# Optimization experiments

Hardware: AMD Instinct MI355X
Metric: run time of the kernel (lower is better)

## Reference

```python
import jax, jax.numpy as jnp
import numpy as np
from jax import lax

B, S, D, H, W = 4, 4096, 512, 8, 32
LL, LG = 4, 3
HD = D // H
SF = 4   # sparsity_factor
K = 7    # depthwise conv kernel


def _ln(x, g, b):
    mu = x.mean(-1, keepdims=True)
    v = ((x - mu) ** 2).mean(-1, keepdims=True)
    return (x - mu) * lax.rsqrt(v + 1e-5) * g + b


def _mha(x, wqkv, bqkv, wp, bp, bias=None):
    Bx, Sx, Dx = x.shape
    qkv = (x @ wqkv + bqkv).reshape(Bx, Sx, 3, H, HD)
    q, k, v = jnp.moveaxis(qkv, 2, 0)          # each [B,S,H,hd]
    att = jnp.einsum('bqhd,bkhd->bhqk', q, k) * (HD ** -0.5)
    if bias is not None:
        att = att + bias                        # relative position bias [1,H,W,W]
    a = jax.nn.softmax(att, axis=-1)
    o = jnp.einsum('bhqk,bkhd->bqhd', a, v).reshape(Bx, Sx, Dx)
    return o @ wp + bp


def _ffn(x, w1, b1, w2, b2):
    return jax.nn.gelu(x @ w1 + b1) @ w2 + b2


def _dwconv(x, w, b):
    # x [B,S,D], w [D,K] depthwise, 'same' padding
    y = lax.conv_general_dilated(
        x.transpose(0, 2, 1), w[:, None, :], (1,), [((K - 1) // 2, (K - 1) // 2)],
        feature_group_count=D, dimension_numbers=('NCH', 'OIH', 'NCH'))
    return (y + b[:, None]).transpose(0, 2, 1)


def _lin_interp(x, L_out):
    # torch F.interpolate(mode='linear', align_corners=False); x [B,Lin,D]
    Lin = x.shape[1]
    pos = jnp.clip((jnp.arange(L_out, dtype=jnp.float32) + 0.5) * (Lin / L_out) - 0.5,
                   0.0, Lin - 1)
    i0 = jnp.floor(pos).astype(jnp.int32)
    i1 = jnp.minimum(i0 + 1, Lin - 1)
    w = (pos - i0)[None, :, None]
    return x[:, i0] * (1.0 - w) + x[:, i1] * w


_rel_idx = np.arange(W)[:, None] - np.arange(W)[None, :] + W - 1   # [W,W]


def _local_attn(x, wqkv, bqkv, wp, bp, rel):
    # Swin-style non-overlapping window attention with relative position bias
    NW = S // W
    bias = rel[_rel_idx].transpose(2, 0, 1)[None]   # [1,H,W,W]
    xw = x.reshape(B * NW, W, D)
    return _mha(xw, wqkv, bqkv, wp, bp, bias).reshape(B, S, D)


def _global_attn(x, wqkv, bqkv, wp, bp):
    # strided sparse global attention + linear interpolation back to S
    if S > SF * 32:
        stride = max(1, S // (SF * 32))
        xs = x[:, ::stride]                         # [B, 128, D]
        return _lin_interp(_mha(xs, wqkv, bqkv, wp, bp), S)
    return _mha(x, wqkv, bqkv, wp, bp)


def _forward(x, p):
    (lqkv_w, lqkv_b, lproj_w, lproj_b, lrel, lconv_w, lconv_b,
     ln1_g, ln1_b, lffn_w1, lffn_b1, lffn_w2, lffn_b2, ln2_g, ln2_b,
     gqkv_w, gqkv_b, gproj_w, gproj_b, gn1_g, gn1_b,
     gffn_w1, gffn_b1, gffn_w2, gffn_b2, gn2_g, gn2_b,
     fw_local, fw_global, fn_g, fn_b) = p
    # local branch: window attention + depthwise conv + FFN, pre-sum/post-norm
    xl = x
    for i in range(LL):
        a = _local_attn(xl, lqkv_w[i], lqkv_b[i], lproj_w[i], lproj_b[i], lrel[i])
        xl = _ln(xl + a, ln1_g[i], ln1_b[i])
        xl = xl + _dwconv(xl, lconv_w[i], lconv_b[i])
        f = _ffn(xl, lffn_w1[i], lffn_b1[i], lffn_w2[i], lffn_b2[i])
        xl = _ln(xl + f, ln2_g[i], ln2_b[i])
    # global branch: sparse strided attention + FFN
    xg = x
    for i in range(LG):
        a = _global_attn(xg, gqkv_w[i], gqkv_b[i], gproj_w[i], gproj_b[i])
        xg = _ln(xg + a, gn1_g[i], gn1_b[i])
        f = _ffn(xg, gffn_w1[i], gffn_b1[i], gffn_w2[i], gffn_b2[i])
        xg = _ln(xg + f, gn2_g[i], gn2_b[i])
    # weighted_sum branch fusion + LayerNorm
    w = jax.nn.softmax(jnp.stack([fw_local, fw_global]))
    return _ln(w[0] * xl + w[1] * xg, fn_g, fn_b)


def setup_inputs() -> dict:
    ks = iter(jax.random.split(jax.random.key(0), 48))
    def r(shape, s=0.02):
        return jax.random.normal(next(ks), shape, dtype=jnp.float32) * s
    return {
        'x': jax.random.normal(next(ks), (B, S, D), dtype=jnp.float32),
        'lqkv_w': r((LL, D, 3 * D)), 'lqkv_b': jnp.zeros((LL, 3 * D)),
        'lproj_w': r((LL, D, D)), 'lproj_b': jnp.zeros((LL, D)),
        'lrel': r((LL, 2 * W - 1, H)),
        'lconv_w': r((LL, D, K)), 'lconv_b': jnp.zeros((LL, D)),
        'ln1_g': jnp.ones((LL, D)), 'ln1_b': jnp.zeros((LL, D)),
        'lffn_w1': r((LL, D, 4 * D)), 'lffn_b1': jnp.zeros((LL, 4 * D)),
        'lffn_w2': r((LL, 4 * D, D)), 'lffn_b2': jnp.zeros((LL, D)),
        'ln2_g': jnp.ones((LL, D)), 'ln2_b': jnp.zeros((LL, D)),
        'gqkv_w': r((LG, D, 3 * D)), 'gqkv_b': jnp.zeros((LG, 3 * D)),
        'gproj_w': r((LG, D, D)), 'gproj_b': jnp.zeros((LG, D)),
        'gn1_g': jnp.ones((LG, D)), 'gn1_b': jnp.zeros((LG, D)),
        'gffn_w1': r((LG, D, 4 * D)), 'gffn_b1': jnp.zeros((LG, 4 * D)),
        'gffn_w2': r((LG, 4 * D, D)), 'gffn_b2': jnp.zeros((LG, D)),
        'gn2_g': jnp.ones((LG, D)), 'gn2_b': jnp.zeros((LG, D)),
        'fw_local': jnp.float32(0.5), 'fw_global': jnp.float32(0.5),
        'fn_g': jnp.ones((D,)), 'fn_b': jnp.zeros((D,)),
    }


def reference(x, lqkv_w, lqkv_b, lproj_w, lproj_b, lrel, lconv_w, lconv_b,
              ln1_g, ln1_b, lffn_w1, lffn_b1, lffn_w2, lffn_b2, ln2_g, ln2_b,
              gqkv_w, gqkv_b, gproj_w, gproj_b, gn1_g, gn1_b,
              gffn_w1, gffn_b1, gffn_w2, gffn_b2, gn2_g, gn2_b,
              fw_local, fw_global, fn_g, fn_b):
    return _forward(x, (lqkv_w, lqkv_b, lproj_w, lproj_b, lrel, lconv_w, lconv_b,
                        ln1_g, ln1_b, lffn_w1, lffn_b1, lffn_w2, lffn_b2, ln2_g, ln2_b,
                        gqkv_w, gqkv_b, gproj_w, gproj_b, gn1_g, gn1_b,
                        gffn_w1, gffn_b1, gffn_w2, gffn_b2, gn2_g, gn2_b,
                        fw_local, fw_global, fn_g, fn_b))
```

## Files before the change

kernel.cpp:

```cpp
#include <hip/hip_runtime.h>
#include <hip/hip_bf16.h>
#include <math.h>

typedef __attribute__((ext_vector_type(8))) short short8;
typedef __attribute__((ext_vector_type(4))) float float4_t;
typedef __attribute__((ext_vector_type(4))) unsigned int uint4_t;
typedef __attribute__((ext_vector_type(2))) unsigned int uint2_t;

#define DEV static __device__ __forceinline__

DEV unsigned short f2b(float f) {
    union { float f; unsigned int u; } x; x.f = f;
    unsigned int r = x.u + 0x7fffu + ((x.u >> 16) & 1u);
    return (unsigned short)(r >> 16);
}
DEV float b2f(unsigned short u) {
    union { unsigned int u; float f; } x; x.u = ((unsigned int)u) << 16;
    return x.f;
}
DEV unsigned int f2b2(float lo, float hi) {
    union { __hip_bfloat162 h; unsigned int u; } c;
    c.h = __float22bfloat162_rn(make_float2(lo, hi));
    return c.u;
}
DEV float gelu_f(float x) {
    const float a = -2.3022082f, b = -0.10294372f;
    float x2 = x * x;
    float p = __builtin_fmaf(x2, b, a);
    float e = __builtin_amdgcn_exp2f(p * x);
    return x * __builtin_amdgcn_rcpf(1.0f + e);
}

DEV void gld16(unsigned short* lds, const unsigned short* g) {
    __builtin_amdgcn_global_load_lds(
        (const __attribute__((address_space(1))) unsigned int*)g,
        (__attribute__((address_space(3))) unsigned int*)lds,
        16, 0, 0);
}

__global__ __launch_bounds__(256) void transpose_cast_batch_kernel(
    const float* __restrict__ srcL, const float* __restrict__ srcG, int nl,
    unsigned short* __restrict__ dst0, size_t perL, int Kd, int Nd)
{
    const int z = blockIdx.z;
    const float* W = (z < nl) ? srcL + (size_t)z * Kd * Nd
                              : srcG + (size_t)(z - nl) * Kd * Nd;
    unsigned short* WT = dst0 + (size_t)z * perL;
    __shared__ float tile[32][33];
    int n0 = blockIdx.x * 32, k0 = blockIdx.y * 32;
    int tx = threadIdx.x & 31, ty = threadIdx.x >> 5;
    #pragma unroll
    for (int r = ty; r < 32; r += 8)
        tile[r][tx] = W[(size_t)(k0 + r) * Nd + n0 + tx];
    __syncthreads();
    #pragma unroll
    for (int r = ty; r < 32; r += 8)
        WT[(size_t)(n0 + r) * Kd + k0 + tx] = f2b(tile[tx][r]);
}

__global__ __launch_bounds__(256) void copy_cast_kernel(
    const float* __restrict__ x, float* __restrict__ xl, float* __restrict__ xg,
    unsigned short* __restrict__ xb, int n4)
{
    int i = blockIdx.x * 256 + threadIdx.x;
    if (i < n4) {
        float4_t v = ((const float4_t*)x)[i];
        ((float4_t*)xl)[i] = v;
        ((float4_t*)xg)[i] = v;
        uint2_t p = { f2b2(v[0], v[1]), f2b2(v[2], v[3]) };
        ((uint2_t*)xb)[i] = p;
    }
}

template<int BN>
__global__ __launch_bounds__(256, 4) void gemm_db_kernel(
    const unsigned short* __restrict__ A,
    const unsigned short* __restrict__ BT,
    const float* __restrict__ bias,
    const float* __restrict__ residual,
    float* __restrict__ Cf,
    unsigned short* __restrict__ Cb,
    int M, int N, int K, int act)
{
    constexpr int NI = (BN == 128) ? 4 : 2;
    __shared__ __align__(16) unsigned short As[2][128 * 32];
    __shared__ __align__(16) unsigned short Bs[2][BN * 32];
    const int tid = threadIdx.x;
    const int wave = tid >> 6, lane = tid & 63;
    const int quad = lane >> 4, l16 = lane & 15;
    const int m0 = blockIdx.x * 128, n0 = blockIdx.y * BN;
    const int wm = (BN == 128) ? (wave >> 1) * 64 : wave * 32;
    const int wn = (BN == 128) ? (wave & 1) * 64 : 0;

    float4_t acc[NI][4] = {};

    const int lrow = lane >> 2;
    const int lcol = (lane & 3) * 8;
    const int r0 = wave * 16 + lrow;
    const unsigned short* Ag0 = A  + (size_t)(m0 + r0) * K + lcol;
    const unsigned short* Ag1 = A  + (size_t)(m0 + 64 + r0) * K + lcol;
    const unsigned short* Bg0 = BT + (size_t)(n0 + r0) * K + lcol;
    const unsigned short* Bg1 = (BN == 128) ? BT + (size_t)(n0 + 64 + r0) * K + lcol : nullptr;
    const int soff = (wave * 16) * 32 + lane * 8;

    const int iters = K >> 5;
    gld16(&As[0][soff], Ag0);
    gld16(&As[0][soff + 64 * 32], Ag1);
    gld16(&Bs[0][soff], Bg0);
    if (BN == 128) gld16(&Bs[0][soff + 64 * 32], Bg1);
    __syncthreads();

    for (int k = 0; k < iters; k++) {
        const int cur = k & 1;
        if (k + 1 < iters) {
            const int koff = (k + 1) << 5;
            const int nxt = cur ^ 1;
            gld16(&As[nxt][soff], Ag0 + koff);
            gld16(&As[nxt][soff + 64 * 32], Ag1 + koff);
            gld16(&Bs[nxt][soff], Bg0 + koff);
            if (BN == 128) gld16(&Bs[nxt][soff + 64 * 32], Bg1 + koff);
        }
        short8 a[NI], b[4];
        #pragma unroll
        for (int i = 0; i < NI; i++)
            a[i] = *(const short8*)(&As[cur][(wm + i * 16 + l16) * 32 + quad * 8]);
        #pragma unroll
        for (int j = 0; j < 4; j++)
            b[j] = *(const short8*)(&Bs[cur][(wn + j * 16 + l16) * 32 + quad * 8]);
        #pragma unroll
        for (int i = 0; i < NI; i++)
            #pragma unroll
            for (int j = 0; j < 4; j++)
                acc[i][j] = __builtin_amdgcn_mfma_f32_16x16x32_bf16(b[j], a[i], acc[i][j], 0, 0, 0);
        __syncthreads();
    }

    #pragma unroll
    for (int i = 0; i < NI; i++) {
        const int row = m0 + wm + i * 16 + l16;
        #pragma unroll
        for (int j = 0; j < 4; j++) {
            const int col = n0 + wn + j * 16 + quad * 4;
            const size_t idx = (size_t)row * N + col;
            float4_t v = acc[i][j] + *(const float4_t*)(bias + col);
            if (act == 1) {
                #pragma unroll
                for (int r = 0; r < 4; r++) v[r] = gelu_f(v[r]);
            }
            if (residual) v += *(const float4_t*)(residual + idx);
            if (Cf) *(float4_t*)(Cf + idx) = v;
            if (Cb) {
                uint2_t o = { f2b2(v[0], v[1]), f2b2(v[2], v[3]) };
                *(uint2_t*)(Cb + idx) = o;
            }
        }
    }
}

__global__ __launch_bounds__(256) void ln_kernel(
    const float* __restrict__ X, const float* __restrict__ g, const float* __restrict__ b,
    float* __restrict__ Yf, unsigned short* __restrict__ Yb)
{
    const int row = blockIdx.x * 4 + (threadIdx.x >> 6);
    const int lane = threadIdx.x & 63;
    const float* xr = X + (size_t)row * 512 + lane * 8;
    float4_t v0 = *(const float4_t*)(xr);
    float4_t v1 = *(const float4_t*)(xr + 4);
    float s = v0[0] + v0[1] + v0[2] + v0[3] + v1[0] + v1[1] + v1[2] + v1[3];
    #pragma unroll
    for (int m = 32; m > 0; m >>= 1) s += __shfl_xor(s, m);
    float mu = s * (1.0f / 512.0f);
    float4_t d0 = v0 - mu, d1 = v1 - mu;
    float s2 = d0[0]*d0[0] + d0[1]*d0[1] + d0[2]*d0[2] + d0[3]*d0[3]
             + d1[0]*d1[0] + d1[1]*d1[1] + d1[2]*d1[2] + d1[3]*d1[3];
    #pragma unroll
    for (int m = 32; m > 0; m >>= 1) s2 += __shfl_xor(s2, m);
    float rs = rsqrtf(s2 * (1.0f / 512.0f) + 1e-5f);
    float4_t g0 = *(const float4_t*)(g + lane * 8);
    float4_t g1 = *(const float4_t*)(g + lane * 8 + 4);
    float4_t b0 = *(const float4_t*)(b + lane * 8);
    float4_t b1 = *(const float4_t*)(b + lane * 8 + 4);
    float4_t y0 = d0 * rs * g0 + b0;
    float4_t y1 = d1 * rs * g1 + b1;
    if (Yf) {
        float* yr = Yf + (size_t)row * 512 + lane * 8;
        *(float4_t*)(yr) = y0;
        *(float4_t*)(yr + 4) = y1;
    }
    if (Yb) {
        uint4_t pk = { f2b2(y0[0], y0[1]), f2b2(y0[2], y0[3]),
                       f2b2(y1[0], y1[1]), f2b2(y1[2], y1[3]) };
        *(uint4_t*)(Yb + (size_t)row * 512 + lane * 8) = pk;
    }
}

__global__ __launch_bounds__(256) void interp_ln_kernel(
    const float* __restrict__ GA, float* __restrict__ XG,
    const float* __restrict__ g, const float* __restrict__ b,
    unsigned short* __restrict__ Yb)
{
    const int row = blockIdx.x * 4 + (threadIdx.x >> 6);
    const int lane = threadIdx.x & 63;
    const int bb = row >> 12, sfull = row & 4095;
    float pos = (sfull + 0.5f) * (128.0f / 4096.0f) - 0.5f;
    pos = fminf(fmaxf(pos, 0.0f), 127.0f);
    int i0 = (int)floorf(pos);
    int i1 = min(i0 + 1, 127);
    float w = pos - (float)i0;
    const float* ga0 = GA + ((size_t)bb * 128 + i0) * 512 + lane * 8;
    const float* ga1 = GA + ((size_t)bb * 128 + i1) * 512 + lane * 8;
    float* xr = XG + (size_t)row * 512 + lane * 8;
    float4_t v0 = *(const float4_t*)(xr)     + *(const float4_t*)(ga0)     * (1.0f - w) + *(const float4_t*)(ga1)     * w;
    float4_t v1 = *(const float4_t*)(xr + 4) + *(const float4_t*)(ga0 + 4) * (1.0f - w) + *(const float4_t*)(ga1 + 4) * w;
    float s = v0[0] + v0[1] + v0[2] + v0[3] + v1[0] + v1[1] + v1[2] + v1[3];
    #pragma unroll
    for (int m = 32; m > 0; m >>= 1) s += __shfl_xor(s, m);
    float mu = s * (1.0f / 512.0f);
    float4_t d0 = v0 - mu, d1 = v1 - mu;
    float s2 = d0[0]*d0[0] + d0[1]*d0[1] + d0[2]*d0[2] + d0[3]*d0[3]
             + d1[0]*d1[0] + d1[1]*d1[1] + d1[2]*d1[2] + d1[3]*d1[3];
    #pragma unroll
    for (int m = 32; m > 0; m >>= 1) s2 += __shfl_xor(s2, m);
    float rs = rsqrtf(s2 * (1.0f / 512.0f) + 1e-5f);
    float4_t g0 = *(const float4_t*)(g + lane * 8);
    float4_t g1 = *(const float4_t*)(g + lane * 8 + 4);
    float4_t b0 = *(const float4_t*)(b + lane * 8);
    float4_t b1 = *(const float4_t*)(b + lane * 8 + 4);
    float4_t y0 = d0 * rs * g0 + b0;
    float4_t y1 = d1 * rs * g1 + b1;
    *(float4_t*)(xr) = y0;
    *(float4_t*)(xr + 4) = y1;
    uint4_t pk = { f2b2(y0[0], y0[1]), f2b2(y0[2], y0[3]),
                   f2b2(y1[0], y1[1]), f2b2(y1[2], y1[3]) };
    *(uint4_t*)(Yb + (size_t)row * 512 + lane * 8) = pk;
}

__global__ __launch_bounds__(256) void local_attn_kernel(
    const unsigned short* __restrict__ QKV, const float* __restrict__ rel,
    unsigned short* __restrict__ OUT)
{
    const int blk = blockIdx.x;
    const int h = blk & 7;
    const int win = (blk >> 3) & 127;
    const int b = blk >> 10;
    const int rowbase = b * 4096 + win * 32;
    __shared__ float q[32][64], k[32][65], v[32][64];
    __shared__ float sc[32][33];
    const int tid = threadIdx.x;
    const int i = tid >> 3, c = tid & 7;
    {
        const unsigned short* base = QKV + (size_t)(rowbase + i) * 1536 + h * 64 + c * 8;
        short8 qv = *(const short8*)(base);
        short8 kv = *(const short8*)(base + 512);
        short8 vv = *(const short8*)(base + 1024);
        #pragma unroll
        for (int r = 0; r < 8; r++) {
            q[i][c * 8 + r] = b2f((unsigned short)qv[r]);
            k[i][c * 8 + r] = b2f((unsigned short)kv[r]);
            v[i][c * 8 + r] = b2f((unsigned short)vv[r]);
        }
    }
    __syncthreads();
    #pragma unroll
    for (int p = 0; p < 4; p++) {
        int idx = tid + p * 256;
        int si = idx >> 5, sj = idx & 31;
        float s = 0.f;
        #pragma unroll
        for (int d = 0; d < 64; d++) s += q[si][d] * k[sj][d];
        sc[si][sj] = s * 0.125f + rel[(si - sj + 31) * 8 + h];
    }
    __syncthreads();
    {
        const int j0 = c * 4;
        float a0 = sc[i][j0], a1 = sc[i][j0 + 1], a2 = sc[i][j0 + 2], a3 = sc[i][j0 + 3];
        float mx = fmaxf(fmaxf(a0, a1), fmaxf(a2, a3));
        #pragma unroll
        for (int m = 1; m < 8; m <<= 1) mx = fmaxf(mx, __shfl_xor(mx, m));
        float e0 = __expf(a0 - mx), e1 = __expf(a1 - mx), e2 = __expf(a2 - mx), e3 = __expf(a3 - mx);
        float sum = e0 + e1 + e2 + e3;
        #pragma unroll
        for (int m = 1; m < 8; m <<= 1) sum += __shfl_xor(sum, m);
        float inv = 1.0f / sum;
        sc[i][j0] = e0 * inv; sc[i][j0 + 1] = e1 * inv; sc[i][j0 + 2] = e2 * inv; sc[i][j0 + 3] = e3 * inv;
    }
    __syncthreads();
    float o[8] = {};
    #pragma unroll
    for (int j = 0; j < 32; j++) {
        float a = sc[i][j];
        #pragma unroll
        for (int r = 0; r < 8; r++) o[r] += a * v[j][c * 8 + r];
    }
    uint4_t pk = { f2b2(o[0], o[1]), f2b2(o[2], o[3]), f2b2(o[4], o[5]), f2b2(o[6], o[7]) };
    *(uint4_t*)(OUT + (size_t)(rowbase + i) * 512 + h * 64 + c * 8) = pk;
}

__global__ __launch_bounds__(256) void gather_xs_kernel(
    const float* __restrict__ XG, unsigned short* __restrict__ XSB)
{
    int i = blockIdx.x * 256 + threadIdx.x;
    if (i < 65536) {
        int dv = (i & 127) * 4, t = (i >> 7) & 127, b = i >> 14;
        float4_t v = *(const float4_t*)(XG + ((size_t)b * 4096 + t * 32) * 512 + dv);
        uint2_t p = { f2b2(v[0], v[1]), f2b2(v[2], v[3]) };
        *(uint2_t*)(XSB + (size_t)i * 4) = p;
    }
}

__global__ __launch_bounds__(256) void global_attn_kernel(
    const unsigned short* __restrict__ GQKV, unsigned short* __restrict__ GOUT)
{
    const int blk = blockIdx.x;
    const int qt = blk & 3, h = (blk >> 2) & 7, b = blk >> 5;
    __shared__ unsigned short ks[128 * 64], vs[128 * 64];
    __shared__ float qs[32 * 64];
    __shared__ float sc[32 * 128];
    const int tid = threadIdx.x;
    for (int idx = tid; idx < 128 * 64; idx += 256) {
        int j = idx >> 6, d = idx & 63;
        const unsigned short* rowp = GQKV + (size_t)(b * 128 + j) * 1536 + h * 64 + d;
        ks[idx] = rowp[512];
        vs[idx] = rowp[1024];
    }
    for (int idx = tid; idx < 32 * 64; idx += 256) {
        int i = idx >> 6, d = idx & 63;
        qs[idx] = b2f(GQKV[(size_t)(b * 128 + qt * 32 + i) * 1536 + h * 64 + d]);
    }
    __syncthreads();
    for (int idx = tid; idx < 32 * 128; idx += 256) {
        int i = idx >> 7, j = idx & 127;
        float s = 0.f;
        #pragma unroll
        for (int d = 0; d < 64; d++) s += qs[i * 64 + d] * b2f(ks[j * 64 + d]);
        sc[idx] = s * 0.125f;
    }
    __syncthreads();
    if (tid < 32) {
        float mx = -1e30f;
        for (int j = 0; j < 128; j++) mx = fmaxf(mx, sc[tid * 128 + j]);
        float sum = 0.f;
        for (int j = 0; j < 128; j++) { float e = __expf(sc[tid * 128 + j] - mx); sc[tid * 128 + j] = e; sum += e; }
        float inv = 1.0f / sum;
        for (int j = 0; j < 128; j++) sc[tid * 128 + j] *= inv;
    }
    __syncthreads();
    for (int idx = tid; idx < 32 * 64; idx += 256) {
        int i = idx >> 6, d = idx & 63;
        float o = 0.f;
        for (int j = 0; j < 128; j++) o += sc[i * 128 + j] * b2f(vs[j * 64 + d]);
        GOUT[(size_t)(b * 128 + qt * 32 + i) * 512 + h * 64 + d] = f2b(o);
    }
}

__global__ __launch_bounds__(256) void dwconv_add_kernel(
    const float* __restrict__ X, const float* __restrict__ wconv, const float* __restrict__ bconv,
    float* __restrict__ Yf, unsigned short* __restrict__ Yb)
{
    __shared__ float wT[7][512];
    const int tid = threadIdx.x;
    for (int idx = tid; idx < 3584; idx += 256) {
        int d = idx / 7, t = idx - d * 7;
        wT[t][d] = wconv[idx];
    }
    __syncthreads();
    const int b = blockIdx.y;
    const int s0 = blockIdx.x * 16 + (tid >> 7) * 8;
    const int dv = (tid & 127) * 4;
    const float* Xb = X + ((size_t)b * 4096) * 512 + dv;

    float4_t win[14];
    #pragma unroll
    for (int j = 0; j < 14; j++) {
        int ss = s0 - 3 + j;
        win[j] = (ss >= 0 && ss < 4096) ? *(const float4_t*)(Xb + (size_t)ss * 512)
                                        : (float4_t){0.f, 0.f, 0.f, 0.f};
    }
    float4_t bias = *(const float4_t*)(bconv + dv);
    float4_t w[7];
    #pragma unroll
    for (int t = 0; t < 7; t++) w[t] = *(const float4_t*)(&wT[t][dv]);

    #pragma unroll
    for (int j = 0; j < 8; j++) {
        float4_t acc = bias;
        #pragma unroll
        for (int t = 0; t < 7; t++) acc += win[j + t] * w[t];
        float4_t v = win[j + 3] + acc;
        size_t e = ((size_t)b * 4096 + s0 + j) * 512 + dv;
        *(float4_t*)(Yf + e) = v;
        uint2_t o = { f2b2(v[0], v[1]), f2b2(v[2], v[3]) };
        *(uint2_t*)(Yb + e) = o;
    }
}

__global__ __launch_bounds__(256) void final_kernel(
    const float* __restrict__ XL, const float* __restrict__ XG,
    const float* __restrict__ fwl, const float* __restrict__ fwg,
    const float* __restrict__ g, const float* __restrict__ bb, float* __restrict__ out)
{
    const int row = blockIdx.x * 4 + (threadIdx.x >> 6);
    const int lane = threadIdx.x & 63;
    float a = fwl[0], cc = fwg[0];
    float m = fmaxf(a, cc);
    float ea = __expf(a - m), ec = __expf(cc - m);
    float w0 = ea / (ea + ec), w1 = ec / (ea + ec);
    const float* xlr = XL + (size_t)row * 512 + lane * 8;
    const float* xgr = XG + (size_t)row * 512 + lane * 8;
    float4_t v0 = *(const float4_t*)(xlr)     * w0 + *(const float4_t*)(xgr)     * w1;
    float4_t v1 = *(const float4_t*)(xlr + 4) * w0 + *(const float4_t*)(xgr + 4) * w1;
    float s = v0[0] + v0[1] + v0[2] + v0[3] + v1[0] + v1[1] + v1[2] + v1[3];
    #pragma unroll
    for (int mm = 32; mm > 0; mm >>= 1) s += __shfl_xor(s, mm);
    float mu = s * (1.0f / 512.0f);
    float4_t d0 = v0 - mu, d1 = v1 - mu;
    float s2 = d0[0]*d0[0] + d0[1]*d0[1] + d0[2]*d0[2] + d0[3]*d0[3]
             + d1[0]*d1[0] + d1[1]*d1[1] + d1[2]*d1[2] + d1[3]*d1[3];
    #pragma unroll
    for (int mm = 32; mm > 0; mm >>= 1) s2 += __shfl_xor(s2, mm);
    float rs = rsqrtf(s2 * (1.0f / 512.0f) + 1e-5f);
    float4_t g0 = *(const float4_t*)(g + lane * 8);
    float4_t g1 = *(const float4_t*)(g + lane * 8 + 4);
    float4_t b0 = *(const float4_t*)(bb + lane * 8);
    float4_t b1 = *(const float4_t*)(bb + lane * 8 + 4);
    float* orow = out + (size_t)row * 512 + lane * 8;
    *(float4_t*)(orow)     = d0 * rs * g0 + b0;
    *(float4_t*)(orow + 4) = d1 * rs * g1 + b1;
}

extern "C" void kernel_launch(void* const* d_in, const int* in_sizes, int n_in,
                              void* d_out, int out_size, void* d_ws, size_t ws_size,
                              hipStream_t stream)
{
    (void)in_sizes; (void)n_in; (void)out_size; (void)ws_size;
    const float* x       = (const float*)d_in[0];
    const float* lqkv_w  = (const float*)d_in[1];
    const float* lqkv_b  = (const float*)d_in[2];
    const float* lproj_w = (const float*)d_in[3];
    const float* lproj_b = (const float*)d_in[4];
    const float* lrel    = (const float*)d_in[5];
    const float* lconv_w = (const float*)d_in[6];
    const float* lconv_b = (const float*)d_in[7];
    const float* ln1_g   = (const float*)d_in[8];
    const float* ln1_b   = (const float*)d_in[9];
    const float* lffn_w1 = (const float*)d_in[10];
    const float* lffn_b1 = (const float*)d_in[11];
    const float* lffn_w2 = (const float*)d_in[12];
    const float* lffn_b2 = (const float*)d_in[13];
    const float* ln2_g   = (const float*)d_in[14];
    const float* ln2_b   = (const float*)d_in[15];
    const float* gqkv_w  = (const float*)d_in[16];
    const float* gqkv_b  = (const float*)d_in[17];
    const float* gproj_w = (const float*)d_in[18];
    const float* gproj_b = (const float*)d_in[19];
    const float* gn1_g   = (const float*)d_in[20];
    const float* gn1_b   = (const float*)d_in[21];
    const float* gffn_w1 = (const float*)d_in[22];
    const float* gffn_b1 = (const float*)d_in[23];
    const float* gffn_w2 = (const float*)d_in[24];
    const float* gffn_b2 = (const float*)d_in[25];
    const float* gn2_g   = (const float*)d_in[26];
    const float* gn2_b   = (const float*)d_in[27];
    const float* fw_local  = (const float*)d_in[28];
    const float* fw_global = (const float*)d_in[29];
    const float* fn_g    = (const float*)d_in[30];
    const float* fn_b    = (const float*)d_in[31];
    float* out = (float*)d_out;

    const int Btot = 4 * 4096;
    const int nel = Btot * 512;

    char* wsb = (char*)d_ws;
    size_t off = 0;
    auto alloc = [&](size_t bytes) -> void* {
        void* p = wsb + off;
        off = (off + bytes + 255) & ~(size_t)255;
        return p;
    };
    float*          XL   = (float*)alloc((size_t)nel * 4);
    float*          XG   = (float*)alloc((size_t)nel * 4);
    float*          TMP  = (float*)alloc((size_t)nel * 4);
    unsigned short* XBl  = (unsigned short*)alloc((size_t)nel * 2);
    unsigned short* XBg  = (unsigned short*)alloc((size_t)nel * 2);
    unsigned short* AOUT = (unsigned short*)alloc((size_t)nel * 2);
    unsigned short* BIG  = (unsigned short*)alloc((size_t)Btot * 2048 * 2);
    unsigned short* WT   = (unsigned short*)alloc((size_t)22020096 * 2);
    unsigned short* XSB  = (unsigned short*)alloc((size_t)512 * 512 * 2);
    unsigned short* GQKV = (unsigned short*)alloc((size_t)512 * 1536 * 2);
    unsigned short* GOUT = (unsigned short*)alloc((size_t)512 * 512 * 2);
    float*          GA   = (float*)alloc((size_t)512 * 512 * 4);

    const size_t perL = 3145728;
    {
        dim3 blk(256);
        transpose_cast_batch_kernel<<<dim3(1536/32, 512/32, 7), blk, 0, stream>>>(
            lqkv_w, gqkv_w, 4, WT, perL, 512, 1536);
        transpose_cast_batch_kernel<<<dim3(512/32, 512/32, 7), blk, 0, stream>>>(
            lproj_w, gproj_w, 4, WT + 786432, perL, 512, 512);
        transpose_cast_batch_kernel<<<dim3(2048/32, 512/32, 7), blk, 0, stream>>>(
            lffn_w1, gffn_w1, 4, WT + 786432 + 262144, perL, 512, 2048);
        transpose_cast_batch_kernel<<<dim3(512/32, 2048/32, 7), blk, 0, stream>>>(
            lffn_w2, gffn_w2, 4, WT + 786432 + 262144 + 1048576, perL, 2048, 512);
    }

    copy_cast_kernel<<<dim3(nel / 1024), dim3(256), 0, stream>>>(x, XL, XG, XBl, nel / 4);

    auto gemm = [&](const unsigned short* A_, const unsigned short* BT_, const float* bias_,
                    const float* res_, float* Cf_, unsigned short* Cb_,
                    int M_, int N_, int K_, int act_) {
        if (N_ >= 1024 || M_ >= 1024) {
            dim3 g(M_ / 128, N_ / 128);
            gemm_db_kernel<128><<<g, dim3(256), 0, stream>>>(A_, BT_, bias_, res_, Cf_, Cb_, M_, N_, K_, act_);
        } else {
            dim3 g(M_ / 128, N_ / 64);
            gemm_db_kernel<64><<<g, dim3(256), 0, stream>>>(A_, BT_, bias_, res_, Cf_, Cb_, M_, N_, K_, act_);
        }
    };

    for (int i = 0; i < 4; i++) {
        unsigned short* base  = WT + (size_t)i * perL;
        unsigned short* qkvT  = base;
        unsigned short* projT = base + 786432;
        unsigned short* w1T   = base + 786432 + 262144;
        unsigned short* w2T   = base + 786432 + 262144 + 1048576;

        gemm(XBl, qkvT, lqkv_b + i * 1536, nullptr, nullptr, BIG, Btot, 1536, 512, 0);
        local_attn_kernel<<<dim3(4096), dim3(256), 0, stream>>>(BIG, lrel + (size_t)i * 63 * 8, AOUT);
        gemm(AOUT, projT, lproj_b + i * 512, XL, TMP, nullptr, Btot, 512, 512, 0);
        ln_kernel<<<dim3(Btot / 4), dim3(256), 0, stream>>>(TMP, ln1_g + i * 512, ln1_b + i * 512, XL, (unsigned short*)nullptr);
        dwconv_add_kernel<<<dim3(256, 4), dim3(256), 0, stream>>>(XL, lconv_w + (size_t)i * 512 * 7, lconv_b + i * 512, TMP, XBl);
        gemm(XBl, w1T, lffn_b1 + i * 2048, nullptr, nullptr, BIG, Btot, 2048, 512, 1);
        gemm(BIG, w2T, lffn_b2 + i * 512, TMP, TMP, nullptr, Btot, 512, 2048, 0);
        ln_kernel<<<dim3(Btot / 4), dim3(256), 0, stream>>>(TMP, ln2_g + i * 512, ln2_b + i * 512, XL, XBl);
    }

    for (int i = 0; i < 3; i++) {
        unsigned short* base  = WT + (size_t)(4 + i) * perL;
        unsigned short* qkvT  = base;
        unsigned short* projT = base + 786432;
        unsigned short* w1T   = base + 786432 + 262144;
        unsigned short* w2T   = base + 786432 + 262144 + 1048576;

        gather_xs_kernel<<<dim3(256), dim3(256), 0, stream>>>(XG, XSB);
        gemm(XSB, qkvT, gqkv_b + i * 1536, nullptr, nullptr, GQKV, 512, 1536, 512, 0);
        global_attn_kernel<<<dim3(128), dim3(256), 0, stream>>>(GQKV, GOUT);
        gemm(GOUT, projT, gproj_b + i * 512, nullptr, GA, nullptr, 512, 512, 512, 0);
        interp_ln_kernel<<<dim3(Btot / 4), dim3(256), 0, stream>>>(GA, XG, gn1_g + i * 512, gn1_b + i * 512, XBg);
        gemm(XBg, w1T, gffn_b1 + i * 2048, nullptr, nullptr, BIG, Btot, 2048, 512, 1);
        gemm(BIG, w2T, gffn_b2 + i * 512, XG, TMP, nullptr, Btot, 512, 2048, 0);
        ln_kernel<<<dim3(Btot / 4), dim3(256), 0, stream>>>(TMP, gn2_g + i * 512, gn2_b + i * 512, XG, XBg);
    }

    final_kernel<<<dim3(Btot / 4), dim3(256), 0, stream>>>(XL, XG, fw_local, fw_global, fn_g, fn_b, out);
}
```

Before: 1.874 ms.

## Split-K the FFN down-projection and fold partial sums into layernorm

The FFN second GEMM (K=2048, N=512) is now split along K into two halves on blockIdx.z, each writing an fp32 partial buffer. A new ln_sum2 kernel adds the two partials, the bias and the residual before the layernorm, so the GEMM epilogue no longer needs them. The GEMM main loop also drops its prefetch double-buffering: each iteration loads two 32-wide K slices, syncs, then computes, and launch bounds rise to 5 blocks per CU. This aims to double the block count of an under-filled GEMM at the cost of extra partial-buffer traffic and less load/compute overlap in every GEMM.

```diff
diff --git a/kernel.cpp b/kernel.cpp
--- a/kernel.cpp
+++ b/kernel.cpp
@@ -73,14 +73,14 @@
 }
 
 template<int BN>
-__global__ __launch_bounds__(256, 4) void gemm_db_kernel(
+__global__ __launch_bounds__(256, 5) void gemm_sb_kernel(
     const unsigned short* __restrict__ A,
     const unsigned short* __restrict__ BT,
     const float* __restrict__ bias,
     const float* __restrict__ residual,
     float* __restrict__ Cf,
     unsigned short* __restrict__ Cb,
-    int M, int N, int K, int act)
+    int M, int N, int Kld, int Kloop, int act)
 {
     constexpr int NI = (BN == 128) ? 4 : 2;
     __shared__ __align__(16) unsigned short As[2][128 * 32];
@@ -89,6 +89,7 @@
     const int wave = tid >> 6, lane = tid & 63;
     const int quad = lane >> 4, l16 = lane & 15;
     const int m0 = blockIdx.x * 128, n0 = blockIdx.y * BN;
+    const int kb = blockIdx.z * Kloop;
     const int wm = (BN == 128) ? (wave >> 1) * 64 : wave * 32;
     const int wn = (BN == 128) ? (wave & 1) * 64 : 0;
 
@@ -97,44 +98,42 @@
     const int lrow = lane >> 2;
     const int lcol = (lane & 3) * 8;
     const int r0 = wave * 16 + lrow;
-    const unsigned short* Ag0 = A  + (size_t)(m0 + r0) * K + lcol;
-    const unsigned short* Ag1 = A  + (size_t)(m0 + 64 + r0) * K + lcol;
-    const unsigned short* Bg0 = BT + (size_t)(n0 + r0) * K + lcol;
-    const unsigned short* Bg1 = (BN == 128) ? BT + (size_t)(n0 + 64 + r0) * K + lcol : nullptr;
+    const unsigned short* Ag0 = A  + (size_t)(m0 + r0) * Kld + kb + lcol;
+    const unsigned short* Ag1 = A  + (size_t)(m0 + 64 + r0) * Kld + kb + lcol;
+    const unsigned short* Bg0 = BT + (size_t)(n0 + r0) * Kld + kb + lcol;
+    const unsigned short* Bg1 = (BN == 128) ? BT + (size_t)(n0 + 64 + r0) * Kld + kb + lcol : nullptr;
     const int soff = (wave * 16) * 32 + lane * 8;
 
-    const int iters = K >> 5;
-    gld16(&As[0][soff], Ag0);
-    gld16(&As[0][soff + 64 * 32], Ag1);
-    gld16(&Bs[0][soff], Bg0);
-    if (BN == 128) gld16(&Bs[0][soff + 64 * 32], Bg1);
-    __syncthreads();
-
-    for (int k = 0; k < iters; k++) {
-        const int cur = k & 1;
-        if (k + 1 < iters) {
-            const int koff = (k + 1) << 5;
-            const int nxt = cur ^ 1;
-            gld16(&As[nxt][soff], Ag0 + koff);
-            gld16(&As[nxt][soff + 64 * 32], Ag1 + koff);
-            gld16(&Bs[nxt][soff], Bg0 + koff);
-            if (BN == 128) gld16(&Bs[nxt][soff + 64 * 32], Bg1 + koff);
+    const int tiles = Kloop >> 6;
+    for (int kt = 0; kt < tiles; kt++) {
+        if (kt) __syncthreads();
+        const int koff = kt << 6;
+        #pragma unroll
+        for (int s = 0; s < 2; s++) {
+            gld16(&As[s][soff],           Ag0 + koff + s * 32);
+            gld16(&As[s][soff + 64 * 32], Ag1 + koff + s * 32);
+            gld16(&Bs[s][soff],           Bg0 + koff + s * 32);
+            if (BN == 128) gld16(&Bs[s][soff + 64 * 32], Bg1 + koff + s * 32);
         }
-        short8 a[NI], b[4];
-        #pragma unroll
-        for (int i = 0; i < NI; i++)
-            a[i] = *(const short8*)(&As[cur][(wm + i * 16 + l16) * 32 + quad * 8]);
-        #pragma unroll
-        for (int j = 0; j < 4; j++)
-            b[j] = *(const short8*)(&Bs[cur][(wn + j * 16 + l16) * 32 + quad * 8]);
-        #pragma unroll
-        for (int i = 0; i < NI; i++)
+        __syncthreads();
+        #pragma unroll
+        for (int s = 0; s < 2; s++) {
+            short8 a[NI], b[4];
+            #pragma unroll
+            for (int i = 0; i < NI; i++)
+                a[i] = *(const short8*)(&As[s][(wm + i * 16 + l16) * 32 + quad * 8]);
             #pragma unroll
             for (int j = 0; j < 4; j++)
-                acc[i][j] = __builtin_amdgcn_mfma_f32_16x16x32_bf16(b[j], a[i], acc[i][j], 0, 0, 0);
-        __syncthreads();
-    }
-
+                b[j] = *(const short8*)(&Bs[s][(wn + j * 16 + l16) * 32 + quad * 8]);
+            #pragma unroll
+            for (int i = 0; i < NI; i++)
+                #pragma unroll
+                for (int j = 0; j < 4; j++)
+                    acc[i][j] = __builtin_amdgcn_mfma_f32_16x16x32_bf16(b[j], a[i], acc[i][j], 0, 0, 0);
+        }
+    }
+
+    float* Cfz = Cf ? Cf + (size_t)blockIdx.z * ((size_t)M * N) : nullptr;
     #pragma unroll
     for (int i = 0; i < NI; i++) {
         const int row = m0 + wm + i * 16 + l16;
@@ -142,13 +141,14 @@
         for (int j = 0; j < 4; j++) {
             const int col = n0 + wn + j * 16 + quad * 4;
             const size_t idx = (size_t)row * N + col;
-            float4_t v = acc[i][j] + *(const float4_t*)(bias + col);
+            float4_t v = acc[i][j];
+            if (bias) v += *(const float4_t*)(bias + col);
             if (act == 1) {
                 #pragma unroll
                 for (int r = 0; r < 4; r++) v[r] = gelu_f(v[r]);
             }
             if (residual) v += *(const float4_t*)(residual + idx);
-            if (Cf) *(float4_t*)(Cf + idx) = v;
+            if (Cfz) *(float4_t*)(Cfz + idx) = v;
             if (Cb) {
                 uint2_t o = { f2b2(v[0], v[1]), f2b2(v[2], v[3]) };
                 *(uint2_t*)(Cb + idx) = o;
@@ -191,6 +191,47 @@
         uint4_t pk = { f2b2(y0[0], y0[1]), f2b2(y0[2], y0[3]),
                        f2b2(y1[0], y1[1]), f2b2(y1[2], y1[3]) };
         *(uint4_t*)(Yb + (size_t)row * 512 + lane * 8) = pk;
+    }
+}
+
+__global__ __launch_bounds__(256) void ln_sum2_kernel(
+    const float* __restrict__ P, long halfn,
+    const float* __restrict__ bias, const float* __restrict__ RES,
+    const float* __restrict__ g, const float* __restrict__ b,
+    float* __restrict__ Yf, unsigned short* __restrict__ Yb)
+{
+    const int row = blockIdx.x * 4 + (threadIdx.x >> 6);
+    const int lane = threadIdx.x & 63;
+    const size_t e = (size_t)row * 512 + lane * 8;
+    float4_t v0 = *(const float4_t*)(P + e) + *(const float4_t*)(P + halfn + e)
+                + *(const float4_t*)(bias + lane * 8) + *(const float4_t*)(RES + e);
+    float4_t v1 = *(const float4_t*)(P + e + 4) + *(const float4_t*)(P + halfn + e + 4)
+                + *(const float4_t*)(bias + lane * 8 + 4) + *(const float4_t*)(RES + e + 4);
+    float s = v0[0] + v0[1] + v0[2] + v0[3] + v1[0] + v1[1] + v1[2] + v1[3];
+    #pragma unroll
+    for (int m = 32; m > 0; m >>= 1) s += __shfl_xor(s, m);
+    float mu = s * (1.0f / 512.0f);
+    float4_t d0 = v0 - mu, d1 = v1 - mu;
+    float s2 = d0[0]*d0[0] + d0[1]*d0[1] + d0[2]*d0[2] + d0[3]*d0[3]
+             + d1[0]*d1[0] + d1[1]*d1[1] + d1[2]*d1[2] + d1[3]*d1[3];
+    #pragma unroll
+    for (int m = 32; m > 0; m >>= 1) s2 += __shfl_xor(s2, m);
+    float rs = rsqrtf(s2 * (1.0f / 512.0f) + 1e-5f);
+    float4_t g0 = *(const float4_t*)(g + lane * 8);
+    float4_t g1 = *(const float4_t*)(g + lane * 8 + 4);
+    float4_t b0 = *(const float4_t*)(b + lane * 8);
+    float4_t b1 = *(const float4_t*)(b + lane * 8 + 4);
+    float4_t y0 = d0 * rs * g0 + b0;
+    float4_t y1 = d1 * rs * g1 + b1;
+    if (Yf) {
+        float* yr = Yf + e;
+        *(float4_t*)(yr) = y0;
+        *(float4_t*)(yr + 4) = y1;
+    }
+    if (Yb) {
+        uint4_t pk = { f2b2(y0[0], y0[1]), f2b2(y0[2], y0[3]),
+                       f2b2(y1[0], y1[1]), f2b2(y1[2], y1[3]) };
+        *(uint4_t*)(Yb + e) = pk;
     }
 }
 
@@ -432,7 +473,7 @@
                               void* d_out, int out_size, void* d_ws, size_t ws_size,
                               hipStream_t stream)
 {
-    (void)in_sizes; (void)n_in; (void)out_size; (void)ws_size;
+    (void)in_sizes; (void)n_in; (void)out_size;
     const float* x       = (const float*)d_in[0];
     const float* lqkv_w  = (const float*)d_in[1];
     const float* lqkv_b  = (const float*)d_in[2];
@@ -489,6 +530,8 @@
     unsigned short* GQKV = (unsigned short*)alloc((size_t)512 * 1536 * 2);
     unsigned short* GOUT = (unsigned short*)alloc((size_t)512 * 512 * 2);
     float*          GA   = (float*)alloc((size_t)512 * 512 * 4);
+    float*          PART = (float*)alloc((size_t)nel * 8);
+    const bool haveP = (off <= ws_size);
 
     const size_t perL = 3145728;
     {
@@ -509,11 +552,11 @@
                     const float* res_, float* Cf_, unsigned short* Cb_,
                     int M_, int N_, int K_, int act_) {
         if (N_ >= 1024 || M_ >= 1024) {
-            dim3 g(M_ / 128, N_ / 128);
-            gemm_db_kernel<128><<<g, dim3(256), 0, stream>>>(A_, BT_, bias_, res_, Cf_, Cb_, M_, N_, K_, act_);
+            dim3 g(M_ / 128, N_ / 128, 1);
+            gemm_sb_kernel<128><<<g, dim3(256), 0, stream>>>(A_, BT_, bias_, res_, Cf_, Cb_, M_, N_, K_, K_, act_);
         } else {
-            dim3 g(M_ / 128, N_ / 64);
-            gemm_db_kernel<64><<<g, dim3(256), 0, stream>>>(A_, BT_, bias_, res_, Cf_, Cb_, M_, N_, K_, act_);
+            dim3 g(M_ / 128, N_ / 64, 1);
+            gemm_sb_kernel<64><<<g, dim3(256), 0, stream>>>(A_, BT_, bias_, res_, Cf_, Cb_, M_, N_, K_, K_, act_);
         }
     };
 
@@ -530,8 +573,15 @@
         ln_kernel<<<dim3(Btot / 4), dim3(256), 0, stream>>>(TMP, ln1_g + i * 512, ln1_b + i * 512, XL, (unsigned short*)nullptr);
         dwconv_add_kernel<<<dim3(256, 4), dim3(256), 0, stream>>>(XL, lconv_w + (size_t)i * 512 * 7, lconv_b + i * 512, TMP, XBl);
         gemm(XBl, w1T, lffn_b1 + i * 2048, nullptr, nullptr, BIG, Btot, 2048, 512, 1);
-        gemm(BIG, w2T, lffn_b2 + i * 512, TMP, TMP, nullptr, Btot, 512, 2048, 0);
-        ln_kernel<<<dim3(Btot / 4), dim3(256), 0, stream>>>(TMP, ln2_g + i * 512, ln2_b + i * 512, XL, XBl);
+        if (haveP) {
+            gemm_sb_kernel<128><<<dim3(Btot / 128, 4, 2), dim3(256), 0, stream>>>(
+                BIG, w2T, nullptr, nullptr, PART, nullptr, Btot, 512, 2048, 1024, 0);
+            ln_sum2_kernel<<<dim3(Btot / 4), dim3(256), 0, stream>>>(
+                PART, (long)nel, lffn_b2 + i * 512, TMP, ln2_g + i * 512, ln2_b + i * 512, XL, XBl);
+        } else {
+            gemm(BIG, w2T, lffn_b2 + i * 512, TMP, TMP, nullptr, Btot, 512, 2048, 0);
+            ln_kernel<<<dim3(Btot / 4), dim3(256), 0, stream>>>(TMP, ln2_g + i * 512, ln2_b + i * 512, XL, XBl);
+        }
     }
 
     for (int i = 0; i < 3; i++) {
@@ -547,8 +597,15 @@
         gemm(GOUT, projT, gproj_b + i * 512, nullptr, GA, nullptr, 512, 512, 512, 0);
         interp_ln_kernel<<<dim3(Btot / 4), dim3(256), 0, stream>>>(GA, XG, gn1_g + i * 512, gn1_b + i * 512, XBg);
         gemm(XBg, w1T, gffn_b1 + i * 2048, nullptr, nullptr, BIG, Btot, 2048, 512, 1);
-        gemm(BIG, w2T, gffn_b2 + i * 512, XG, TMP, nullptr, Btot, 512, 2048, 0);
-        ln_kernel<<<dim3(Btot / 4), dim3(256), 0, stream>>>(TMP, gn2_g + i * 512, gn2_b + i * 512, XG, XBg);
+        if (haveP) {
+            gemm_sb_kernel<128><<<dim3(Btot / 128, 4, 2), dim3(256), 0, stream>>>(
+                BIG, w2T, nullptr, nullptr, PART, nullptr, Btot, 512, 2048, 1024, 0);
+            ln_sum2_kernel<<<dim3(Btot / 4), dim3(256), 0, stream>>>(
+                PART, (long)nel, gffn_b2 + i * 512, XG, gn2_g + i * 512, gn2_b + i * 512, XG, XBg);
+        } else {
+            gemm(BIG, w2T, gffn_b2 + i * 512, XG, TMP, nullptr, Btot, 512, 2048, 0);
+            ln_kernel<<<dim3(Btot / 4), dim3(256), 0, stream>>>(TMP, gn2_g + i * 512, gn2_b + i * 512, XG, XBg);
+        }
     }
 
     final_kernel<<<dim3(Btot / 4), dim3(256), 0, stream>>>(XL, XG, fw_local, fw_global, fn_g, fn_b, out);
```

Result: slower. 2.419 ms (+29.1%).
